# Performance work log

Measured on AMD Instinct MI355X. Metric: run time of the kernel, lower is better.

## Reference

```python
import jax, jax.numpy as jnp
import numpy as np

HIDDEN_N = 6
B, C, H, W = 16, 4, 512, 512


def _make_filters():
    identity = jnp.array([[0., 0., 0.], [0., 1., 0.], [0., 0., 0.]], jnp.float32)
    sobel_x = jnp.array([[-1., 0., 1.], [-2., 0., 2.], [-1., 0., 1.]], jnp.float32)
    lap = jnp.array([[1., 2., 1.], [2., -12., 2.], [1., 2., 1.]], jnp.float32)
    # [4, 3, 3]: identity, sobel_x, sobel_y (= sobel_x.T), laplacian
    return jnp.stack([identity, sobel_x, sobel_x.T, lap])


def setup_inputs() -> dict:
    key = jax.random.key(0)
    ks = jax.random.split(key, 6)
    x = jax.random.normal(ks[0], (B, C, H, W), jnp.float32)
    filters = _make_filters()
    # Conv2d(16, hidden_n, 1): weight [hidden_n, 16], kaiming-uniform-like init
    s1 = 1.0 / np.sqrt(16.0)
    w1_w = jax.random.uniform(ks[1], (HIDDEN_N, 16), jnp.float32, -s1, s1)
    w1_b = jax.random.uniform(ks[2], (HIDDEN_N,), jnp.float32, -s1, s1)
    s2 = 1.0 / np.sqrt(float(HIDDEN_N))
    # zero_w2=True: w2 weight zeroed at init (bias kept random)
    w2_w = jnp.zeros((4, HIDDEN_N), jnp.float32)
    w2_b = jax.random.uniform(ks[3], (4,), jnp.float32, -s2, s2)
    w3_w = jax.random.uniform(ks[4], (4, HIDDEN_N), jnp.float32, -s2, s2)
    w3_b = jax.random.uniform(ks[5], (4,), jnp.float32, -s2, s2)
    return {"x": x, "filters": filters, "w1_w": w1_w, "w1_b": w1_b,
            "w2_w": w2_w, "w2_b": w2_b, "w3_w": w3_w, "w3_b": w3_b}


def _perchannel_conv(x, filters):
    # x: [B, C, H, W], filters: [4, 3, 3] -> [B, C*4, H, W] (channel-major, filter-minor)
    b, c, h, w = x.shape
    xp = jnp.pad(x, ((0, 0), (0, 0), (1, 1), (1, 1)), mode="wrap")  # circular pad
    lhs = xp.reshape(b * c, 1, h + 2, w + 2)
    y = jax.lax.conv_general_dilated(
        lhs, filters[:, None], window_strides=(1, 1), padding="VALID",
        dimension_numbers=("NCHW", "OIHW", "NCHW"))  # [b*c, 4, h, w]
    return y.reshape(b, c * 4, h, w)


def _conv1x1(h, w, b):
    # 1x1 conv == channel contraction
    return jnp.einsum("bchw,oc->bohw", h, w) + b[None, :, None, None]


def reference(x, filters, w1_w, w1_b, w2_w, w2_b, w3_w, w3_b):
    y = _perchannel_conv(x, filters)                     # [B, 16, H, W]
    hid = jax.nn.relu(_conv1x1(y, w1_w, w1_b))           # [B, 6, H, W]
    y_upd = jnp.tanh(_conv1x1(hid, w2_w, w2_b))          # [B, 4, H, W]
    gate = jax.nn.sigmoid(_conv1x1(hid, w3_w, w3_b))     # [B, 4, H, W]
    return x * gate + (1.0 - gate) * y_upd
```

## Files before the change

### kernel.cpp

```cpp
#include <hip/hip_runtime.h>


constexpr int Bn = 16, Cn = 4, Hn = 512, Wn = 512, HID = 6;

__device__ __forceinline__ float frcp(float v) { return __builtin_amdgcn_rcpf(v); }

__global__ __launch_bounds__(256, 4) void nca_row2(
    const float* __restrict__ x,
    const float* __restrict__ w1w, const float* __restrict__ w1b,
    const float* __restrict__ w2w, const float* __restrict__ w2b,
    const float* __restrict__ w3w, const float* __restrict__ w3b,
    float* __restrict__ out)
{
    const int lane = threadIdx.x & 63;
    const int wv   = threadIdx.x >> 6;
    const int row = __builtin_amdgcn_readfirstlane((int)blockIdx.x * 4 + wv);
    const int h  = row & (Hn - 1);
    const int b  = row >> 9;
    const int hm = (h - 1) & (Hn - 1);
    const int hp = (h + 1) & (Hn - 1);

    const int w0 = lane << 3;
    const int laneL = (lane + 63) & 63;
    const int laneR = (lane + 1) & 63;

    const size_t plane = (size_t)Hn * Wn;
    const float* xb = x + (size_t)b * Cn * plane;

    float acc[HID][8];
    #pragma unroll
    for (int o = 0; o < HID; ++o) {
        float bv = w1b[o];
        #pragma unroll
        for (int i = 0; i < 8; ++i) acc[o][i] = bv;
    }

    #pragma unroll
    for (int c = 0; c < Cn; ++c) {
        const float* rt = xb + c * plane + (size_t)hm * Wn;
        const float* rm = xb + c * plane + (size_t)h  * Wn;
        const float* rb = xb + c * plane + (size_t)hp * Wn;
        float4 t0 = *(const float4*)(rt + w0), t1 = *(const float4*)(rt + w0 + 4);
        float4 m0 = *(const float4*)(rm + w0), m1 = *(const float4*)(rm + w0 + 4);
        float4 b0 = *(const float4*)(rb + w0), b1 = *(const float4*)(rb + w0 + 4);

        float m[8] = { m0.x, m0.y, m0.z, m0.w, m1.x, m1.y, m1.z, m1.w };
        float s[8], d[8];
        {
            float t[8] = { t0.x, t0.y, t0.z, t0.w, t1.x, t1.y, t1.z, t1.w };
            float q[8] = { b0.x, b0.y, b0.z, b0.w, b1.x, b1.y, b1.z, b1.w };
            #pragma unroll
            for (int j = 0; j < 8; ++j) {
                s[j] = fmaf(2.f, m[j], t[j] + q[j]);
                d[j] = q[j] - t[j];
            }
        }

        float sL = __shfl(s[7], laneL), dL = __shfl(d[7], laneL);
        float sR = __shfl(s[0], laneR), dR = __shfl(d[0], laneR);

        #pragma unroll
        for (int i = 0; i < 8; ++i) {
            float sm = (i == 0) ? sL : s[i - 1];
            float sp = (i == 7) ? sR : s[i + 1];
            float dm = (i == 0) ? dL : d[i - 1];
            float dp = (i == 7) ? dR : d[i + 1];
            float mc = m[i];
            float y1 = sp - sm;
            float y2 = fmaf(2.f, d[i], dm + dp);
            float y3 = fmaf(-16.f, mc, fmaf(2.f, s[i], sm + sp));
            #pragma unroll
            for (int o = 0; o < HID; ++o) {
                acc[o][i] = fmaf(w1w[o*16 + c*4 + 0], mc,
                            fmaf(w1w[o*16 + c*4 + 1], y1,
                            fmaf(w1w[o*16 + c*4 + 2], y2,
                            fmaf(w1w[o*16 + c*4 + 3], y3, acc[o][i]))));
            }
        }
    }

    #pragma unroll
    for (int o = 0; o < HID; ++o)
        #pragma unroll
        for (int i = 0; i < 8; ++i)
            acc[o][i] = fmaxf(acc[o][i], 0.f);

    float* ob = out + (size_t)b * Cn * plane + (size_t)h * Wn;
    #pragma unroll
    for (int j = 0; j < Cn; ++j) {
        const float* rc = xb + j * plane + (size_t)h * Wn;
        float4 c0 = *(const float4*)(rc + w0), c1 = *(const float4*)(rc + w0 + 4);
        float xc[8] = { c0.x, c0.y, c0.z, c0.w, c1.x, c1.y, c1.z, c1.w };
        float res[8];
        #pragma unroll
        for (int i = 0; i < 8; ++i) {
            float u = w2b[j], gg = w3b[j];
            #pragma unroll
            for (int o = 0; o < HID; ++o) {
                u  = fmaf(w2w[j*HID + o], acc[o][i], u);
                gg = fmaf(w3w[j*HID + o], acc[o][i], gg);
            }
            float th = 1.f - 2.f * frcp(__expf(2.f * u) + 1.f);
            float sg = frcp(1.f + __expf(-gg));
            res[i] = fmaf(sg, xc[i] - th, th);
        }
        *(float4*)(ob + j * plane + w0)     = make_float4(res[0], res[1], res[2], res[3]);
        *(float4*)(ob + j * plane + w0 + 4) = make_float4(res[4], res[5], res[6], res[7]);
    }
}

extern "C" void kernel_launch(void* const* d_in, const int* in_sizes, int n_in,
                              void* d_out, int out_size, void* d_ws, size_t ws_size,
                              hipStream_t stream) {
    const float* x   = (const float*)d_in[0];
    const float* w1w = (const float*)d_in[2];
    const float* w1b = (const float*)d_in[3];
    const float* w2w = (const float*)d_in[4];
    const float* w2b = (const float*)d_in[5];
    const float* w3w = (const float*)d_in[6];
    const float* w3b = (const float*)d_in[7];
    float* out = (float*)d_out;

    int rows   = Bn * Hn;
    int blocks = rows / 4;
    nca_row2<<<blocks, 256, 0, stream>>>(x, w1w, w1b, w2w, w2b, w3w, w3b, out);
}
```

Baseline: 166.4 us.

## Split each row across two waves with 4 pixels per lane and halo fetch

Each wavefront now processes half a row, 256 columns, at 4 pixels per lane instead of a full row at 8 pixels per lane. This doubles the wave count and roughly halves register pressure per thread. The edge lanes fetch the halo column directly with scalar loads, and the center pixels are reused from the stencil loads instead of being reloaded for the output blend. The min-waves launch bound is also dropped. In exchange there are extra halo loads, more redundant row fetches, and narrower per-lane memory transactions.

```diff
diff --git a/kernel.cpp b/kernel.cpp
--- a/kernel.cpp
+++ b/kernel.cpp
@@ -5,7 +5,7 @@
 
 __device__ __forceinline__ float frcp(float v) { return __builtin_amdgcn_rcpf(v); }
 
-__global__ __launch_bounds__(256, 4) void nca_row2(
+__global__ __launch_bounds__(256) void nca_half(
     const float* __restrict__ x,
     const float* __restrict__ w1w, const float* __restrict__ w1b,
     const float* __restrict__ w2w, const float* __restrict__ w2b,
@@ -13,62 +13,75 @@
     float* __restrict__ out)
 {
     const int lane = threadIdx.x & 63;
-    const int wv   = threadIdx.x >> 6;
-    const int row = __builtin_amdgcn_readfirstlane((int)blockIdx.x * 4 + wv);
-    const int h  = row & (Hn - 1);
-    const int b  = row >> 9;
+    const int wid = __builtin_amdgcn_readfirstlane((int)blockIdx.x * 4 + (threadIdx.x >> 6));
+    const int half = wid & 1;
+    const int h    = (wid >> 1) & (Hn - 1);
+    const int b    = wid >> 10;
     const int hm = (h - 1) & (Hn - 1);
     const int hp = (h + 1) & (Hn - 1);
 
-    const int w0 = lane << 3;
+    const int W0 = half << 8;
+    const int w0 = W0 + (lane << 2);
+
+    const int colL = (W0 - 1) & (Wn - 1);
+    const int colR = (W0 + 256) & (Wn - 1);
+    const int colFix = (lane == 0) ? colL : colR;
     const int laneL = (lane + 63) & 63;
     const int laneR = (lane + 1) & 63;
 
     const size_t plane = (size_t)Hn * Wn;
     const float* xb = x + (size_t)b * Cn * plane;
 
-    float acc[HID][8];
+    float acc[HID][4];
     #pragma unroll
     for (int o = 0; o < HID; ++o) {
         float bv = w1b[o];
         #pragma unroll
-        for (int i = 0; i < 8; ++i) acc[o][i] = bv;
+        for (int i = 0; i < 4; ++i) acc[o][i] = bv;
     }
+
+    float xc[Cn][4];
 
     #pragma unroll
     for (int c = 0; c < Cn; ++c) {
         const float* rt = xb + c * plane + (size_t)hm * Wn;
         const float* rm = xb + c * plane + (size_t)h  * Wn;
         const float* rb = xb + c * plane + (size_t)hp * Wn;
-        float4 t0 = *(const float4*)(rt + w0), t1 = *(const float4*)(rt + w0 + 4);
-        float4 m0 = *(const float4*)(rm + w0), m1 = *(const float4*)(rm + w0 + 4);
-        float4 b0 = *(const float4*)(rb + w0), b1 = *(const float4*)(rb + w0 + 4);
+        float4 t4 = *(const float4*)(rt + w0);
+        float4 m4 = *(const float4*)(rm + w0);
+        float4 q4 = *(const float4*)(rb + w0);
+        float tF = rt[colFix], mF = rm[colFix], qF = rb[colFix];
 
-        float m[8] = { m0.x, m0.y, m0.z, m0.w, m1.x, m1.y, m1.z, m1.w };
-        float s[8], d[8];
+        float m[4] = { m4.x, m4.y, m4.z, m4.w };
+        float s[4], d[4];
         {
-            float t[8] = { t0.x, t0.y, t0.z, t0.w, t1.x, t1.y, t1.z, t1.w };
-            float q[8] = { b0.x, b0.y, b0.z, b0.w, b1.x, b1.y, b1.z, b1.w };
+            float t[4] = { t4.x, t4.y, t4.z, t4.w };
+            float q[4] = { q4.x, q4.y, q4.z, q4.w };
             #pragma unroll
-            for (int j = 0; j < 8; ++j) {
+            for (int j = 0; j < 4; ++j) {
                 s[j] = fmaf(2.f, m[j], t[j] + q[j]);
                 d[j] = q[j] - t[j];
             }
         }
+        float sF = fmaf(2.f, mF, tF + qF);
+        float dF = qF - tF;
 
-        float sL = __shfl(s[7], laneL), dL = __shfl(d[7], laneL);
+        float sL = __shfl(s[3], laneL), dL = __shfl(d[3], laneL);
         float sR = __shfl(s[0], laneR), dR = __shfl(d[0], laneR);
+        sL = (lane == 0) ? sF : sL;  dL = (lane == 0) ? dF : dL;
+        sR = (lane == 63) ? sF : sR; dR = (lane == 63) ? dF : dR;
 
         #pragma unroll
-        for (int i = 0; i < 8; ++i) {
+        for (int i = 0; i < 4; ++i) {
             float sm = (i == 0) ? sL : s[i - 1];
-            float sp = (i == 7) ? sR : s[i + 1];
+            float sp = (i == 3) ? sR : s[i + 1];
             float dm = (i == 0) ? dL : d[i - 1];
-            float dp = (i == 7) ? dR : d[i + 1];
+            float dp = (i == 3) ? dR : d[i + 1];
             float mc = m[i];
             float y1 = sp - sm;
             float y2 = fmaf(2.f, d[i], dm + dp);
             float y3 = fmaf(-16.f, mc, fmaf(2.f, s[i], sm + sp));
+            xc[c][i] = mc;
             #pragma unroll
             for (int o = 0; o < HID; ++o) {
                 acc[o][i] = fmaf(w1w[o*16 + c*4 + 0], mc,
@@ -82,18 +95,15 @@
     #pragma unroll
     for (int o = 0; o < HID; ++o)
         #pragma unroll
-        for (int i = 0; i < 8; ++i)
+        for (int i = 0; i < 4; ++i)
             acc[o][i] = fmaxf(acc[o][i], 0.f);
 
-    float* ob = out + (size_t)b * Cn * plane + (size_t)h * Wn;
+    float* ob = out + (size_t)b * Cn * plane + (size_t)h * Wn + w0;
     #pragma unroll
     for (int j = 0; j < Cn; ++j) {
-        const float* rc = xb + j * plane + (size_t)h * Wn;
-        float4 c0 = *(const float4*)(rc + w0), c1 = *(const float4*)(rc + w0 + 4);
-        float xc[8] = { c0.x, c0.y, c0.z, c0.w, c1.x, c1.y, c1.z, c1.w };
-        float res[8];
+        float res[4];
         #pragma unroll
-        for (int i = 0; i < 8; ++i) {
+        for (int i = 0; i < 4; ++i) {
             float u = w2b[j], gg = w3b[j];
             #pragma unroll
             for (int o = 0; o < HID; ++o) {
@@ -102,10 +112,9 @@
             }
             float th = 1.f - 2.f * frcp(__expf(2.f * u) + 1.f);
             float sg = frcp(1.f + __expf(-gg));
-            res[i] = fmaf(sg, xc[i] - th, th);
+            res[i] = fmaf(sg, xc[j][i] - th, th);
         }
-        *(float4*)(ob + j * plane + w0)     = make_float4(res[0], res[1], res[2], res[3]);
-        *(float4*)(ob + j * plane + w0 + 4) = make_float4(res[4], res[5], res[6], res[7]);
+        *(float4*)(ob + (size_t)j * plane) = make_float4(res[0], res[1], res[2], res[3]);
     }
 }
 
@@ -121,7 +130,7 @@
     const float* w3b = (const float*)d_in[7];
     float* out = (float*)d_out;
 
-    int rows   = Bn * Hn;
-    int blocks = rows / 4;
-    nca_row2<<<blocks, 256, 0, stream>>>(x, w1w, w1b, w2w, w2b, w3w, w3b, out);
+    int waves  = Bn * Hn * 2;
+    int blocks = waves / 4;
+    nca_half<<<blocks, 256, 0, stream>>>(x, w1w, w1b, w2w, w2b, w3w, w3b, out);
 }
```

Measured after the change: 133.6 us. 19.8% less time.
